# Kernel optimization log

Measured on AMD Instinct MI355X. Metric: run time of the kernel, lower is better.

## Reference

```python
import jax, jax.numpy as jnp
import numpy as np

C = 64


def setup_inputs() -> dict:
    key = jax.random.key(0)
    ks = jax.random.split(key, 7)
    x = jax.random.normal(ks[0], (8, C, 64, 64), dtype=jnp.float32)
    # 1x1 conv weights stored as [out_c, in_c]; biases [out_c]
    s = 1.0 / np.sqrt(C)
    W1 = jax.random.uniform(ks[1], (C, C), jnp.float32, -s, s)
    b1 = jax.random.uniform(ks[2], (C,), jnp.float32, -s, s)
    W2 = jax.random.uniform(ks[3], (C, C), jnp.float32, -s, s)
    b2 = jax.random.uniform(ks[4], (C,), jnp.float32, -s, s)
    W3 = jax.random.uniform(ks[5], (C, C), jnp.float32, -s, s)
    b3 = jax.random.uniform(ks[6], (C,), jnp.float32, -s, s)
    return {"x": x, "W1": W1, "b1": b1, "W2": W2, "b2": b2, "W3": W3, "b3": b3}


def reference(x, W1, b1, W2, b2, W3, b3):
    gamma = 1.0
    b, c, h, w = x.shape
    xf = x.reshape(b, c, h * w)  # [b, c, n]
    # 1x1 convs == per-pixel channel matmuls
    f = jnp.einsum('oc,bcn->bon', W1, xf) + b1[None, :, None]
    g = jnp.einsum('oc,bcn->bon', W2, xf) + b2[None, :, None]
    k = jnp.einsum('oc,bcn->bon', W3, xf) + b3[None, :, None]
    # scores[b,i,j] = sum_c f[b,c,i] * g[b,c,j]; softmax over j
    scores = jnp.einsum('bci,bcj->bij', f, g)
    attn = jax.nn.softmax(scores, axis=2)
    # out_attn[b,c,i] = sum_j attn[b,i,j] * k[b,c,j]
    out = jnp.einsum('bij,bcj->bci', attn, k).reshape(b, c, h, w)
    return gamma * out + x
```

## Files before the change

### kernel.cpp

```cpp
#include <hip/hip_runtime.h>
#include <hip/hip_bf16.h>

#define NPIX 4096
#define CCH  64
#define NB   8
#define KVBLK 64

typedef __attribute__((ext_vector_type(8)))  short short8;
typedef __attribute__((ext_vector_type(4)))  float f32x4;
typedef __attribute__((ext_vector_type(16))) float f32x16;

#define LOG2E   1.44269504f

__global__ __launch_bounds__(256) void proj_kernel(
    const float* __restrict__ x,
    const float* __restrict__ W1, const float* __restrict__ b1,
    const float* __restrict__ W2, const float* __restrict__ b2,
    const float* __restrict__ W3, const float* __restrict__ b3,
    __hip_bfloat16* __restrict__ Q, __hip_bfloat16* __restrict__ G,
    __hip_bfloat16* __restrict__ K)
{
    const int m    = blockIdx.x % 3;
    const int tile = blockIdx.x / 3;
    const int b    = tile >> 6;
    const int i0   = (tile & 63) << 6;

    const float* W  = (m == 0) ? W1 : (m == 1) ? W2 : W3;
    const float* bv = (m == 0) ? b1 : (m == 1) ? b2 : b3;

    __shared__ float xs[64][65];
    __shared__ float Wt[64][68];

    for (int e = threadIdx.x; e < 4096; e += 256) {
        const int c = e >> 6, p = e & 63;
        xs[c][p] = x[(size_t)b * CCH * NPIX + (size_t)c * NPIX + i0 + p];
        Wt[e & 63][e >> 6] = W[e];
    }
    __syncthreads();

    const int p = threadIdx.x & 63;
    const int g = threadIdx.x >> 6;

    float acc[16];
    #pragma unroll
    for (int oo = 0; oo < 16; ++oo) acc[oo] = bv[g * 16 + oo];

    for (int c = 0; c < 64; ++c) {
        const float xv = xs[c][p];
        const f32x4* w = (const f32x4*)&Wt[c][g * 16];
        #pragma unroll
        for (int qq = 0; qq < 4; ++qq) {
            const f32x4 a = w[qq];
            #pragma unroll
            for (int j = 0; j < 4; ++j)
                acc[qq * 4 + j] += a[j] * xv;
        }
    }

    const int i = i0 + p;
    if (m == 0) {
        #pragma unroll
        for (int oo = 0; oo < 16; ++oo)
            Q[(size_t)b * NPIX * CCH + (size_t)i * CCH + g * 16 + oo] =
                __float2bfloat16(acc[oo] * LOG2E);
    } else if (m == 1) {
        #pragma unroll
        for (int oo = 0; oo < 16; ++oo)
            G[(size_t)b * NPIX * CCH + (size_t)i * CCH + g * 16 + oo] =
                __float2bfloat16(acc[oo]);
    } else {
        #pragma unroll
        for (int oo = 0; oo < 16; ++oo)
            K[(size_t)b * CCH * NPIX + (size_t)(g * 16 + oo) * NPIX + i] =
                __float2bfloat16(acc[oo]);
    }
}

__device__ __forceinline__ void gload_lds16(const void* g, void* l) {
    __builtin_amdgcn_global_load_lds(
        (const __attribute__((address_space(1))) unsigned int*)g,
        (__attribute__((address_space(3))) unsigned int*)l, 16, 0, 0);
}
__device__ __forceinline__ unsigned int pack_bf16(float lo, float hi) {
    union { __hip_bfloat162 h; unsigned int u; } w;
    w.h = __float22bfloat162_rn(make_float2(lo, hi));
    return w.u;
}

__global__ __launch_bounds__(512, 4) void attn_kernel(
    const __hip_bfloat16* __restrict__ Qg, const __hip_bfloat16* __restrict__ Gg,
    const __hip_bfloat16* __restrict__ Kg,
    __hip_bfloat16* __restrict__ Opart, float* __restrict__ Lpart, int split)
{
    __shared__ char lds[2][16384];

    const int blk   = blockIdx.x;
    const int per_b = 16 * split;
    const int b     = blk / per_b;
    const int rem   = blk - b * per_b;
    const int itile = rem / split;
    const int sp    = rem - itile * split;
    const int tid   = threadIdx.x;
    const int wave  = tid >> 6;
    const int lane  = tid & 63;
    const int l32   = lane & 31;
    const int hi    = lane >> 5;
    const int i0w   = itile * 256 + wave * 32;
    const int jcnt  = NPIX / split;
    const int jlo   = sp * jcnt;
    const int niter = jcnt / KVBLK;

    const short* Qb = (const short*)Qg + (size_t)b * NPIX * CCH;
    const char*  Gb = (const char*)(Gg + (size_t)b * NPIX * CCH);
    const char*  Kb = (const char*)(Kg + (size_t)b * CCH * NPIX);

    short8 q[4];
    #pragma unroll
    for (int ks = 0; ks < 4; ++ks)
        q[ks] = *(const short8*)(Qb + (size_t)(i0w + l32) * CCH + ks * 16 + hi * 8);

    int gbase[2], kbase[2];
    #pragma unroll
    for (int jb = 0; jb < 2; ++jb)
        gbase[jb] = (jb * 32 + l32) * 128 + ((l32 & 7) << 4);
    #pragma unroll
    for (int cb = 0; cb < 2; ++cb)
        kbase[cb] = 8192 + (cb * 32 + l32) * 128 + ((l32 & 7) << 4);

    const int srow = tid >> 3, scolb = (tid & 7) * 16;
    const char* gsrc = Gb + (size_t)(jlo + srow) * 128 + (scolb ^ ((srow & 7) << 4));
    const char* ksrc = Kb + (size_t)srow * 8192 + (size_t)jlo * 2 + (scolb ^ ((srow & 7) << 4));

    f32x16 zacc;
    #pragma unroll
    for (int r = 0; r < 16; ++r) zacc[r] = 0.f;

    f32x16 o[2];
    #pragma unroll
    for (int cb = 0; cb < 2; ++cb)
        #pragma unroll
        for (int r = 0; r < 16; ++r) o[cb][r] = 0.f;
    float ps = 0.f;

    auto STAGE = [&](int buf, int tt) {
        gload_lds16(gsrc + tt * (KVBLK * 128), lds[buf] + wave * 1024);
        gload_lds16(ksrc + tt * (KVBLK * 2),  lds[buf] + 8192 + wave * 1024);
    };

    STAGE(0, 0);
    __syncthreads();

    for (int t = 0; t < niter; ++t) {
        const int cur = t & 1;
        STAGE(cur ^ 1, (t + 1 < niter) ? t + 1 : 0);
        const char* L = lds[cur];

        #pragma unroll
        for (int jb = 0; jb < 2; ++jb) {
            short8 ga[4];
            #pragma unroll
            for (int ks = 0; ks < 4; ++ks)
                ga[ks] = *(const short8*)(L + (gbase[jb] ^ ((2 * ks + hi) << 4)));

            __builtin_amdgcn_s_setprio(1);
            f32x16 acc = __builtin_amdgcn_mfma_f32_32x32x16_bf16(ga[0], q[0], zacc, 0, 0, 0);
            acc = __builtin_amdgcn_mfma_f32_32x32x16_bf16(ga[1], q[1], acc, 0, 0, 0);
            acc = __builtin_amdgcn_mfma_f32_32x32x16_bf16(ga[2], q[2], acc, 0, 0, 0);
            acc = __builtin_amdgcn_mfma_f32_32x32x16_bf16(ga[3], q[3], acc, 0, 0, 0);
            __builtin_amdgcn_s_setprio(0);

            float p[16];
            #pragma unroll
            for (int r = 0; r < 16; ++r) {
                p[r] = __builtin_amdgcn_exp2f(acc[r]);
                ps += p[r];
            }
            short8 pf[2];
            #pragma unroll
            for (int kk = 0; kk < 2; ++kk) {
                unsigned int x0 = pack_bf16(p[8 * kk + 0], p[8 * kk + 1]);
                unsigned int x1 = pack_bf16(p[8 * kk + 2], p[8 * kk + 3]);
                unsigned int y0 = pack_bf16(p[8 * kk + 4], p[8 * kk + 5]);
                unsigned int y1 = pack_bf16(p[8 * kk + 6], p[8 * kk + 7]);
                asm("v_permlane32_swap_b32 %0, %1" : "+v"(x0), "+v"(y0));
                asm("v_permlane32_swap_b32 %0, %1" : "+v"(x1), "+v"(y1));
                union { unsigned int u[4]; short8 v; } w;
                w.u[0] = x0; w.u[1] = x1; w.u[2] = y0; w.u[3] = y1;
                pf[kk] = w.v;
            }

            __builtin_amdgcn_s_setprio(1);
            #pragma unroll
            for (int kk = 0; kk < 2; ++kk) {
                const int ksg = 2 * jb + kk;
                const short8 ka0 = *(const short8*)(L + (kbase[0] ^ ((2 * ksg + hi) << 4)));
                const short8 ka1 = *(const short8*)(L + (kbase[1] ^ ((2 * ksg + hi) << 4)));
                o[0] = __builtin_amdgcn_mfma_f32_32x32x16_bf16(ka0, pf[kk], o[0], 0, 0, 0);
                o[1] = __builtin_amdgcn_mfma_f32_32x32x16_bf16(ka1, pf[kk], o[1], 0, 0, 0);
            }
            __builtin_amdgcn_s_setprio(0);
        }
        __syncthreads();
    }

    const size_t pb = (size_t)(b * split + sp);
    #pragma unroll
    for (int cb = 0; cb < 2; ++cb)
        #pragma unroll
        for (int r = 0; r < 16; ++r) {
            const int c = cb * 32 + (r & 3) + 8 * (r >> 2) + 4 * hi;
            const int i = i0w + l32;
            Opart[(pb * CCH + c) * NPIX + i] = __float2bfloat16(o[cb][r]);
        }
    ps += __shfl_xor(ps, 32);
    if (lane < 32)
        Lpart[pb * NPIX + i0w + l32] = ps;
}

__global__ __launch_bounds__(256) void combine_kernel(
    const __hip_bfloat16* __restrict__ Opart, const float* __restrict__ Lpart,
    const float* __restrict__ x, float* __restrict__ out, int split)
{
    const int b = blockIdx.x >> 6, c = blockIdx.x & 63;
    #pragma unroll
    for (int chunk = 0; chunk < 2; ++chunk) {
        const int i = chunk * 2048 + threadIdx.x * 8;
        float acc[8] = {0,0,0,0,0,0,0,0};
        float Ls[8]  = {0,0,0,0,0,0,0,0};
        for (int s = 0; s < split; ++s) {
            const size_t pb = (size_t)(b * split + s);
            const short8 ov = *(const short8*)((const short*)Opart + (pb * CCH + c) * NPIX + i);
            const f32x4 l0 = *(const f32x4*)&Lpart[pb * NPIX + i];
            const f32x4 l1 = *(const f32x4*)&Lpart[pb * NPIX + i + 4];
            #pragma unroll
            for (int t = 0; t < 8; ++t) {
                union { unsigned int u; float f; } cv;
                cv.u = ((unsigned int)(unsigned short)ov[t]) << 16;
                acc[t] += cv.f;
                Ls[t]  += (t < 4) ? l0[t] : l1[t - 4];
            }
        }
        const size_t idx = ((size_t)b * CCH + c) * NPIX + i;
        const f32x4 xv0 = *(const f32x4*)&x[idx];
        const f32x4 xv1 = *(const f32x4*)&x[idx + 4];
        f32x4 r0, r1;
        #pragma unroll
        for (int t = 0; t < 4; ++t) {
            r0[t] = acc[t] / Ls[t] + xv0[t];
            r1[t] = acc[t + 4] / Ls[t + 4] + xv1[t];
        }
        *(f32x4*)&out[idx]     = r0;
        *(f32x4*)&out[idx + 4] = r1;
    }
}

extern "C" void kernel_launch(void* const* d_in, const int* in_sizes, int n_in,
                              void* d_out, int out_size, void* d_ws, size_t ws_size,
                              hipStream_t stream) {
    const float* x  = (const float*)d_in[0];
    const float* W1 = (const float*)d_in[1];
    const float* b1 = (const float*)d_in[2];
    const float* W2 = (const float*)d_in[3];
    const float* b2 = (const float*)d_in[4];
    const float* W3 = (const float*)d_in[5];
    const float* b3 = (const float*)d_in[6];
    float* out = (float*)d_out;

    char* ws = (char*)d_ws;
    const size_t planeB = (size_t)NB * NPIX * CCH * sizeof(__hip_bfloat16);
    __hip_bfloat16* Q = (__hip_bfloat16*)(ws);
    __hip_bfloat16* G = (__hip_bfloat16*)(ws + planeB);
    __hip_bfloat16* K = (__hip_bfloat16*)(ws + 2 * planeB);

    const size_t base   = 3 * planeB;
    const size_t oPlane = planeB;
    const size_t lPlane = (size_t)NB * NPIX * sizeof(float);

    int split = 8;
    while (split > 1 && base + (size_t)split * (oPlane + lPlane) > ws_size)
        split >>= 1;

    __hip_bfloat16* Opart = (__hip_bfloat16*)(ws + base);
    float* Lpart = (float*)(ws + base + (size_t)split * oPlane);

    proj_kernel<<<dim3(NB * 64 * 3), dim3(256), 0, stream>>>(x, W1, b1, W2, b2, W3, b3, Q, G, K);
    attn_kernel<<<dim3(NB * 16 * split), dim3(512), 0, stream>>>(Q, G, K, Opart, Lpart, split);
    combine_kernel<<<dim3(NB * CCH), dim3(256), 0, stream>>>(Opart, Lpart, x, out, split);
}
```

Baseline: 82.09 us.

## Interleave score MFMAs across both key blocks and precompute inverse softmax sums

The attention loop now loads both key-block fragments up front and interleaves the two independent MFMA accumulation chains, so the two dependency chains can hide each other's latency. The per-(batch, channel) combine kernel no longer re-reads and re-sums the softmax denominators for every channel. A new small kernel sums them once per pixel and writes reciprocals into the workspace, which the combine kernel multiplies by. This costs an extra kernel launch and more live registers in the attention loop, and invL reuses workspace memory that held Q.

```diff
diff --git a/kernel.cpp b/kernel.cpp
--- a/kernel.cpp
+++ b/kernel.cpp
@@ -155,20 +155,26 @@
         STAGE(cur ^ 1, (t + 1 < niter) ? t + 1 : 0);
         const char* L = lds[cur];
 
+        short8 ga0[4], ga1[4];
+        #pragma unroll
+        for (int ks = 0; ks < 4; ++ks) {
+            ga0[ks] = *(const short8*)(L + (gbase[0] ^ ((2 * ks + hi) << 4)));
+            ga1[ks] = *(const short8*)(L + (gbase[1] ^ ((2 * ks + hi) << 4)));
+        }
+        __builtin_amdgcn_s_setprio(1);
+        f32x16 acc0 = __builtin_amdgcn_mfma_f32_32x32x16_bf16(ga0[0], q[0], zacc, 0, 0, 0);
+        f32x16 acc1 = __builtin_amdgcn_mfma_f32_32x32x16_bf16(ga1[0], q[0], zacc, 0, 0, 0);
+        acc0 = __builtin_amdgcn_mfma_f32_32x32x16_bf16(ga0[1], q[1], acc0, 0, 0, 0);
+        acc1 = __builtin_amdgcn_mfma_f32_32x32x16_bf16(ga1[1], q[1], acc1, 0, 0, 0);
+        acc0 = __builtin_amdgcn_mfma_f32_32x32x16_bf16(ga0[2], q[2], acc0, 0, 0, 0);
+        acc1 = __builtin_amdgcn_mfma_f32_32x32x16_bf16(ga1[2], q[2], acc1, 0, 0, 0);
+        acc0 = __builtin_amdgcn_mfma_f32_32x32x16_bf16(ga0[3], q[3], acc0, 0, 0, 0);
+        acc1 = __builtin_amdgcn_mfma_f32_32x32x16_bf16(ga1[3], q[3], acc1, 0, 0, 0);
+        __builtin_amdgcn_s_setprio(0);
+
         #pragma unroll
         for (int jb = 0; jb < 2; ++jb) {
-            short8 ga[4];
-            #pragma unroll
-            for (int ks = 0; ks < 4; ++ks)
-                ga[ks] = *(const short8*)(L + (gbase[jb] ^ ((2 * ks + hi) << 4)));
-
-            __builtin_amdgcn_s_setprio(1);
-            f32x16 acc = __builtin_amdgcn_mfma_f32_32x32x16_bf16(ga[0], q[0], zacc, 0, 0, 0);
-            acc = __builtin_amdgcn_mfma_f32_32x32x16_bf16(ga[1], q[1], acc, 0, 0, 0);
-            acc = __builtin_amdgcn_mfma_f32_32x32x16_bf16(ga[2], q[2], acc, 0, 0, 0);
-            acc = __builtin_amdgcn_mfma_f32_32x32x16_bf16(ga[3], q[3], acc, 0, 0, 0);
-            __builtin_amdgcn_s_setprio(0);
-
+            const f32x16& acc = jb ? acc1 : acc0;
             float p[16];
             #pragma unroll
             for (int r = 0; r < 16; ++r) {
@@ -217,8 +223,19 @@
         Lpart[pb * NPIX + i0w + l32] = ps;
 }
 
+__global__ __launch_bounds__(1024) void lsum_kernel(
+    const float* __restrict__ Lpart, float* __restrict__ invL, int split)
+{
+    const int idx = blockIdx.x * 1024 + threadIdx.x;
+    const int b = idx >> 12, i = idx & 4095;
+    float L = 0.f;
+    for (int s = 0; s < split; ++s)
+        L += Lpart[((size_t)(b * split + s)) * NPIX + i];
+    invL[idx] = 1.0f / L;
+}
+
 __global__ __launch_bounds__(256) void combine_kernel(
-    const __hip_bfloat16* __restrict__ Opart, const float* __restrict__ Lpart,
+    const __hip_bfloat16* __restrict__ Opart, const float* __restrict__ invL,
     const float* __restrict__ x, float* __restrict__ out, int split)
 {
     const int b = blockIdx.x >> 6, c = blockIdx.x & 63;
@@ -226,28 +243,27 @@
     for (int chunk = 0; chunk < 2; ++chunk) {
         const int i = chunk * 2048 + threadIdx.x * 8;
         float acc[8] = {0,0,0,0,0,0,0,0};
-        float Ls[8]  = {0,0,0,0,0,0,0,0};
         for (int s = 0; s < split; ++s) {
             const size_t pb = (size_t)(b * split + s);
             const short8 ov = *(const short8*)((const short*)Opart + (pb * CCH + c) * NPIX + i);
-            const f32x4 l0 = *(const f32x4*)&Lpart[pb * NPIX + i];
-            const f32x4 l1 = *(const f32x4*)&Lpart[pb * NPIX + i + 4];
             #pragma unroll
             for (int t = 0; t < 8; ++t) {
                 union { unsigned int u; float f; } cv;
                 cv.u = ((unsigned int)(unsigned short)ov[t]) << 16;
                 acc[t] += cv.f;
-                Ls[t]  += (t < 4) ? l0[t] : l1[t - 4];
             }
         }
+        const size_t li = (size_t)b * NPIX + i;
+        const f32x4 il0 = *(const f32x4*)&invL[li];
+        const f32x4 il1 = *(const f32x4*)&invL[li + 4];
         const size_t idx = ((size_t)b * CCH + c) * NPIX + i;
         const f32x4 xv0 = *(const f32x4*)&x[idx];
         const f32x4 xv1 = *(const f32x4*)&x[idx + 4];
         f32x4 r0, r1;
         #pragma unroll
         for (int t = 0; t < 4; ++t) {
-            r0[t] = acc[t] / Ls[t] + xv0[t];
-            r1[t] = acc[t + 4] / Ls[t + 4] + xv1[t];
+            r0[t] = acc[t] * il0[t] + xv0[t];
+            r1[t] = acc[t + 4] * il1[t] + xv1[t];
         }
         *(f32x4*)&out[idx]     = r0;
         *(f32x4*)&out[idx + 4] = r1;
@@ -282,8 +298,10 @@
 
     __hip_bfloat16* Opart = (__hip_bfloat16*)(ws + base);
     float* Lpart = (float*)(ws + base + (size_t)split * oPlane);
+    float* invL  = (float*)(ws);
 
     proj_kernel<<<dim3(NB * 64 * 3), dim3(256), 0, stream>>>(x, W1, b1, W2, b2, W3, b3, Q, G, K);
     attn_kernel<<<dim3(NB * 16 * split), dim3(512), 0, stream>>>(Q, G, K, Opart, Lpart, split);
-    combine_kernel<<<dim3(NB * CCH), dim3(256), 0, stream>>>(Opart, Lpart, x, out, split);
-}
+    lsum_kernel<<<dim3(NB * NPIX / 1024), dim3(1024), 0, stream>>>(Lpart, invL, split);
+    combine_kernel<<<dim3(NB * CCH), dim3(256), 0, stream>>>(Opart, invL, x, out, split);
+}
```

Measured after the change: 85.56 us. 1.04x slower.

## Triple-buffer attention KV staging with partial vmcnt wait; restructure combine kernel

Applied to the files above, without the earlier changes.

The attention kernel moves from double to triple LDS buffering. It prefetches two tiles ahead and replaces __syncthreads with a barrier that waits only until at most two loads are outstanding (vmcnt(2)), so global-to-LDS loads overlap more compute. The combine kernel is reorganised so each block handles a 64-pixel tile across all channels. It computes the inverse softmax denominators once in shared memory and multiplies instead of dividing per element. Triple buffering raises LDS use to 48KB per block, which may reduce occupancy at 4 blocks per CU.

```diff
diff --git a/kernel.cpp b/kernel.cpp
--- a/kernel.cpp
+++ b/kernel.cpp
@@ -86,13 +86,19 @@
     w.h = __float22bfloat162_rn(make_float2(lo, hi));
     return w.u;
 }
+__device__ __forceinline__ void pipe_barrier() {
+    asm volatile("s_waitcnt vmcnt(2)" ::: "memory");
+    __builtin_amdgcn_sched_barrier(0);
+    __builtin_amdgcn_s_barrier();
+    __builtin_amdgcn_sched_barrier(0);
+}
 
 __global__ __launch_bounds__(512, 4) void attn_kernel(
     const __hip_bfloat16* __restrict__ Qg, const __hip_bfloat16* __restrict__ Gg,
     const __hip_bfloat16* __restrict__ Kg,
     __hip_bfloat16* __restrict__ Opart, float* __restrict__ Lpart, int split)
 {
-    __shared__ char lds[2][16384];
+    __shared__ char lds[3][16384];
 
     const int blk   = blockIdx.x;
     const int per_b = 16 * split;
@@ -148,11 +154,13 @@
     };
 
     STAGE(0, 0);
-    __syncthreads();
-
+    STAGE(1, 1);
+    pipe_barrier();
+
+    int cur = 0;
     for (int t = 0; t < niter; ++t) {
-        const int cur = t & 1;
-        STAGE(cur ^ 1, (t + 1 < niter) ? t + 1 : 0);
+        const int nxt2 = (cur == 0) ? 2 : (cur == 1) ? 0 : 1;
+        STAGE(nxt2, (t + 2 < niter) ? t + 2 : 0);
         const char* L = lds[cur];
 
         #pragma unroll
@@ -200,7 +208,8 @@
             }
             __builtin_amdgcn_s_setprio(0);
         }
-        __syncthreads();
+        pipe_barrier();
+        cur = (cur == 2) ? 0 : cur + 1;
     }
 
     const size_t pb = (size_t)(b * split + sp);
@@ -221,36 +230,49 @@
     const __hip_bfloat16* __restrict__ Opart, const float* __restrict__ Lpart,
     const float* __restrict__ x, float* __restrict__ out, int split)
 {
-    const int b = blockIdx.x >> 6, c = blockIdx.x & 63;
-    #pragma unroll
-    for (int chunk = 0; chunk < 2; ++chunk) {
-        const int i = chunk * 2048 + threadIdx.x * 8;
-        float acc[8] = {0,0,0,0,0,0,0,0};
-        float Ls[8]  = {0,0,0,0,0,0,0,0};
-        for (int s = 0; s < split; ++s) {
-            const size_t pb = (size_t)(b * split + s);
-            const short8 ov = *(const short8*)((const short*)Opart + (pb * CCH + c) * NPIX + i);
-            const f32x4 l0 = *(const f32x4*)&Lpart[pb * NPIX + i];
-            const f32x4 l1 = *(const f32x4*)&Lpart[pb * NPIX + i + 4];
-            #pragma unroll
-            for (int t = 0; t < 8; ++t) {
-                union { unsigned int u; float f; } cv;
-                cv.u = ((unsigned int)(unsigned short)ov[t]) << 16;
-                acc[t] += cv.f;
-                Ls[t]  += (t < 4) ? l0[t] : l1[t - 4];
-            }
+    const int b  = blockIdx.x >> 6;
+    const int i0 = (blockIdx.x & 63) << 6;
+
+    __shared__ float invL[64];
+    if (threadIdx.x < 64) {
+        const int i = i0 + threadIdx.x;
+        float L = 0.f;
+        for (int s = 0; s < split; ++s)
+            L += Lpart[((size_t)(b * split + s)) * NPIX + i];
+        invL[threadIdx.x] = 1.0f / L;
+    }
+    __syncthreads();
+
+    const int c    = threadIdx.x >> 2;
+    const int ioff = (threadIdx.x & 3) * 16;
+
+    float acc[16];
+    #pragma unroll
+    for (int k = 0; k < 16; ++k) acc[k] = 0.f;
+
+    for (int s = 0; s < split; ++s) {
+        const size_t base = (((size_t)(b * split + s)) * CCH + c) * NPIX + i0 + ioff;
+        const short8 v0 = *(const short8*)((const short*)Opart + base);
+        const short8 v1 = *(const short8*)((const short*)Opart + base + 8);
+        #pragma unroll
+        for (int k = 0; k < 8; ++k) {
+            union { unsigned int u; float f; } cv0, cv1;
+            cv0.u = ((unsigned int)(unsigned short)v0[k]) << 16;
+            cv1.u = ((unsigned int)(unsigned short)v1[k]) << 16;
+            acc[k]     += cv0.f;
+            acc[k + 8] += cv1.f;
         }
-        const size_t idx = ((size_t)b * CCH + c) * NPIX + i;
-        const f32x4 xv0 = *(const f32x4*)&x[idx];
-        const f32x4 xv1 = *(const f32x4*)&x[idx + 4];
-        f32x4 r0, r1;
-        #pragma unroll
-        for (int t = 0; t < 4; ++t) {
-            r0[t] = acc[t] / Ls[t] + xv0[t];
-            r1[t] = acc[t + 4] / Ls[t + 4] + xv1[t];
-        }
-        *(f32x4*)&out[idx]     = r0;
-        *(f32x4*)&out[idx + 4] = r1;
+    }
+
+    const size_t idx = ((size_t)b * CCH + c) * NPIX + i0 + ioff;
+    #pragma unroll
+    for (int kq = 0; kq < 4; ++kq) {
+        const f32x4 xv = *(const f32x4*)&x[idx + 4 * kq];
+        f32x4 r;
+        #pragma unroll
+        for (int t = 0; t < 4; ++t)
+            r[t] = acc[kq * 4 + t] * invL[ioff + kq * 4 + t] + xv[t];
+        *(f32x4*)&out[idx + 4 * kq] = r;
     }
 }
 
@@ -285,5 +307,5 @@
 
     proj_kernel<<<dim3(NB * 64 * 3), dim3(256), 0, stream>>>(x, W1, b1, W2, b2, W3, b3, Q, G, K);
     attn_kernel<<<dim3(NB * 16 * split), dim3(512), 0, stream>>>(Q, G, K, Opart, Lpart, split);
-    combine_kernel<<<dim3(NB * CCH), dim3(256), 0, stream>>>(Opart, Lpart, x, out, split);
-}
+    combine_kernel<<<dim3(NB * 64), dim3(256), 0, stream>>>(Opart, Lpart, x, out, split);
+}
```

New measurement: 83.32 us. About the same (+1.5%).
